# Optimization experiments

Hardware: AMD Instinct MI355X
Metric: run time of the kernel (lower is better)

The kernel has to match this reference:

```python
import jax, jax.numpy as jnp
import numpy as np

HEADS = 8
DIM_HEAD = 64
SCALE = 10.0
EPS = 1e-12  # F.normalize eps


def setup_inputs() -> dict:
    key = jax.random.key(0)
    k1, k2, k3, k4 = jax.random.split(key, 4)
    dim, hidden = 256, HEADS * DIM_HEAD
    x = jax.random.normal(k1, (8, dim, 32, 32), dtype=jnp.float32)
    w_qkv = jax.random.normal(k2, (3 * hidden, dim), dtype=jnp.float32) * (1.0 / np.sqrt(dim))
    w_out = jax.random.normal(k3, (dim, hidden), dtype=jnp.float32) * (1.0 / np.sqrt(hidden))
    b_out = jax.random.normal(k4, (dim,), dtype=jnp.float32) * 0.01
    return {"x": x, "w_qkv": w_qkv, "w_out": w_out, "b_out": b_out}


def _l2norm_last(t):
    # matches F.normalize(t, dim=-1): t / max(||t||_2, eps)
    n = jnp.sqrt(jnp.sum(t * t, axis=-1, keepdims=True))
    return t / jnp.maximum(n, EPS)


def reference(x, w_qkv, w_out, b_out):
    b, c, hh, ww = x.shape
    n = hh * ww
    # 1x1 conv == channel matmul
    qkv = jnp.einsum('bcxy,oc->boxy', x, w_qkv)  # (b, 3*hidden, h, w)
    q, k, v = jnp.split(qkv, 3, axis=1)
    # 'b (h c) x y -> b h c (x y)'
    to_heads = lambda t: t.reshape(b, HEADS, DIM_HEAD, n)
    q, k, v = to_heads(q), to_heads(k), to_heads(v)
    # NOTE: l2norm over the LAST axis = spatial token axis n (faithful to source)
    q = _l2norm_last(q)
    k = _l2norm_last(k)
    sim = jnp.einsum('bhdi,bhdj->bhij', q, k) * SCALE  # (b, h, n, n)
    attn = jax.nn.softmax(sim, axis=-1)
    out = jnp.einsum('bhij,bhdj->bhid', attn, v)  # (b, h, n, d)
    # 'b h (x y) d -> b (h d) x y'
    out = out.transpose(0, 1, 3, 2).reshape(b, HEADS * DIM_HEAD, hh, ww)
    return jnp.einsum('bcxy,oc->boxy', out, w_out) + b_out[None, :, None, None]
```

## Files before the change

kernel.cpp:

```cpp
#include <hip/hip_runtime.h>
#include <math.h>

#define NHEADS 8
#define DHEAD  64
#define HIDDEN 512
#define CIN    256
#define NTOK   1024
#define QK_SCALE 10.0f
#define LOG2E 1.44269504088896f
#define MSHIFT 10.5f
#define MBIAS  (-MSHIFT * LOG2E)

typedef __bf16 bf16x8 __attribute__((ext_vector_type(8)));
typedef float  f32x4  __attribute__((ext_vector_type(4)));
typedef unsigned u32x4 __attribute__((ext_vector_type(4)));
typedef unsigned short u16x8 __attribute__((ext_vector_type(8)));
typedef unsigned short u16x4 __attribute__((ext_vector_type(4)));

__device__ inline unsigned short f2bf(float f) {
    unsigned u = __builtin_bit_cast(unsigned, f);
    u = (u + 0x7FFFu + ((u >> 16) & 1u)) >> 16;
    return (unsigned short)u;
}

__device__ inline unsigned pk2(float a, float b) {
    return (unsigned)f2bf(a) | ((unsigned)f2bf(b) << 16);
}

__device__ inline unsigned pk2t(float a, float b) {
    return (__builtin_bit_cast(unsigned, a) >> 16) |
           (__builtin_bit_cast(unsigned, b) & 0xFFFF0000u);
}
__device__ inline float trunc_bf(float f) {
    return __builtin_bit_cast(float, __builtin_bit_cast(unsigned, f) & 0xFFFF0000u);
}

__device__ inline float bf2f(unsigned short u) {
    return __builtin_bit_cast(float, (unsigned)u << 16);
}

__device__ inline bf16x8 cvt8(const float* p) {
    float4 a = *(const float4*)p;
    float4 b = *(const float4*)(p + 4);
    u16x8 t;
    t[0] = f2bf(a.x); t[1] = f2bf(a.y); t[2] = f2bf(a.z); t[3] = f2bf(a.w);
    t[4] = f2bf(b.x); t[5] = f2bf(b.y); t[6] = f2bf(b.z); t[7] = f2bf(b.w);
    return __builtin_bit_cast(bf16x8, t);
}

__global__ __launch_bounds__(256)
void cvt_x_kernel(const float* __restrict__ x, unsigned short* __restrict__ xt) {
    const int b  = blockIdx.z;
    const int c0 = blockIdx.y * 64;
    const int n0 = blockIdx.x * 64;
    const float* src = x + ((size_t)b * CIN + c0) * NTOK + n0;
    unsigned short* dst = xt + ((size_t)b * NTOK + n0) * CIN + c0;

    __shared__ float T[64][65];
    const int t = threadIdx.x;
    {
        const int nq = t & 15, cg = t >> 4;
        #pragma unroll
        for (int rr = 0; rr < 4; ++rr) {
            const int c = cg + rr * 16;
            float4 v = *(const float4*)(src + (size_t)c * NTOK + nq * 4);
            T[c][nq * 4 + 0] = v.x;
            T[c][nq * 4 + 1] = v.y;
            T[c][nq * 4 + 2] = v.z;
            T[c][nq * 4 + 3] = v.w;
        }
    }
    __syncthreads();
    {
        const int n = t >> 2, cq = t & 3;
        alignas(16) unsigned short tmp[16];
        #pragma unroll
        for (int e = 0; e < 16; ++e)
            tmp[e] = f2bf(T[cq * 16 + e][n]);
        *(uint4*)(dst + (size_t)n * CIN + cq * 16)     = *(uint4*)&tmp[0];
        *(uint4*)(dst + (size_t)n * CIN + cq * 16 + 8) = *(uint4*)&tmp[8];
    }
}

__global__ __launch_bounds__(256)
void cvt_w_kernel(const float* __restrict__ wq, const float* __restrict__ wo,
                  unsigned short* __restrict__ wqb, unsigned short* __restrict__ wob) {
    const size_t i = ((size_t)blockIdx.x * 256 + threadIdx.x) * 8;
    if (i < (size_t)1536 * 256) {
        *(bf16x8*)(wqb + i) = cvt8(wq + i);
    } else {
        const size_t j = i - (size_t)1536 * 256;
        *(bf16x8*)(wob + j) = cvt8(wo + j);
    }
}

__global__ __launch_bounds__(256)
void gemm1_kernel(const unsigned short* __restrict__ wqb,
                  const unsigned short* __restrict__ xt,
                  float* __restrict__ qt,
                  unsigned short* __restrict__ vb,
                  float* __restrict__ ss) {
    const int b  = blockIdx.z;
    const int bm = blockIdx.y * 128;
    const int bn = blockIdx.x * 128;
    const int wave = threadIdx.x >> 6, lane = threadIdx.x & 63;
    const int lo = lane & 15, hi = lane >> 4;
    const int wm = bm + (wave >> 1) * 64;
    const int wn = bn + (wave & 1) * 64;

    const unsigned short* Ab = wqb + (size_t)(wm + lo) * CIN + hi * 8;
    const unsigned short* Bb = xt + ((size_t)b * NTOK + wn + lo) * CIN + hi * 8;

    f32x4 acc[4][4];
    #pragma unroll
    for (int mi = 0; mi < 4; ++mi)
        #pragma unroll
        for (int ni = 0; ni < 4; ++ni) acc[mi][ni] = (f32x4){0.f, 0.f, 0.f, 0.f};

    for (int k0 = 0; k0 < CIN; k0 += 32) {
        bf16x8 a[4], bf[4];
        #pragma unroll
        for (int mi = 0; mi < 4; ++mi) a[mi]  = *(const bf16x8*)(Ab + (size_t)mi * 16 * CIN + k0);
        #pragma unroll
        for (int ni = 0; ni < 4; ++ni) bf[ni] = *(const bf16x8*)(Bb + (size_t)ni * 16 * CIN + k0);
        #pragma unroll
        for (int mi = 0; mi < 4; ++mi)
            #pragma unroll
            for (int ni = 0; ni < 4; ++ni)
                acc[mi][ni] = __builtin_amdgcn_mfma_f32_16x16x32_bf16(a[mi], bf[ni], acc[mi][ni], 0, 0, 0);
    }

    __shared__ unsigned short VL[4][32][72];

    if (bm < 1024) {
        const int isK = (wm >= 512) ? 1 : 0;
        const int ch0 = wm & 511;
        const int head = ch0 >> 6;
        float* dst = qt + (((size_t)isK * 64 + b * 8 + head) * NTOK) * DHEAD;
        #pragma unroll
        for (int mi = 0; mi < 4; ++mi) {
            const int d = mi * 16 + hi * 4;
            #pragma unroll
            for (int ni = 0; ni < 4; ++ni) {
                const int n = wn + ni * 16 + lo;
                *(f32x4*)(dst + (size_t)n * DHEAD + d) = acc[mi][ni];
            }
        }
        float p[4][4];
        #pragma unroll
        for (int mi = 0; mi < 4; ++mi)
            #pragma unroll
            for (int r = 0; r < 4; ++r) {
                float s = 0.f;
                #pragma unroll
                for (int ni = 0; ni < 4; ++ni) s += acc[mi][ni][r] * acc[mi][ni][r];
                p[mi][r] = s;
            }
        #pragma unroll
        for (int off = 1; off < 16; off <<= 1)
            #pragma unroll
            for (int mi = 0; mi < 4; ++mi)
                #pragma unroll
                for (int r = 0; r < 4; ++r)
                    p[mi][r] += __shfl_xor(p[mi][r], off, 64);
        if (lo == 0) {
            #pragma unroll
            for (int mi = 0; mi < 4; ++mi)
                #pragma unroll
                for (int r = 0; r < 4; ++r)
                    atomicAdd(&ss[(size_t)b * 1024 + isK * 512 + ch0 + mi * 16 + hi * 4 + r], p[mi][r]);
        }
    } else {
        const int ch0 = wm - 1024;
        const int h = ch0 >> 6;
        unsigned short* tile = vb + (((size_t)b * 8 + h) * 16 + (wn >> 6)) * 4096;
        #pragma unroll
        for (int half = 0; half < 2; ++half) {
            #pragma unroll
            for (int mm = 0; mm < 2; ++mm) {
                const int mi = half * 2 + mm;
                #pragma unroll
                for (int ni = 0; ni < 4; ++ni)
                    #pragma unroll
                    for (int r = 0; r < 4; ++r)
                        VL[wave][mm * 16 + hi * 4 + r][ni * 16 + lo] = f2bf(acc[mi][ni][r]);
            }
            #pragma unroll
            for (int i = 0; i < 4; ++i) {
                const int flat = i * 64 + lane;
                const int row = flat >> 3, c = flat & 7;
                const int tb = c >> 2, hg = c & 3;
                const uint2 vlo = *(uint2*)&VL[wave][row][tb * 32 + hg * 4];
                const uint2 vhi = *(uint2*)&VL[wave][row][tb * 32 + hg * 4 + 16];
                uint4 v = make_uint4(vlo.x, vlo.y, vhi.x, vhi.y);
                const int d = half * 32 + row;
                *(uint4*)(tile + (size_t)d * 64 + c * 8) = v;
            }
        }
    }
}

__global__ __launch_bounds__(256)
void scale_cvt_kernel(const float* __restrict__ qt, const float* __restrict__ ss,
                      unsigned short* __restrict__ qs, unsigned short* __restrict__ ks) {
    const size_t idx = ((size_t)blockIdx.x * 256 + threadIdx.x) * 8;
    const size_t half = (size_t)64 * NTOK * DHEAD;
    const int isK = idx >= half;
    const size_t rem = idx - (size_t)isK * half;
    const int bh = (int)(rem >> 16);
    const int d0 = (int)(rem & 63);
    const int b  = bh >> 3;
    const int ch = isK * 512 + (bh & 7) * 64 + d0;
    const float scl = isK ? 1.0f : QK_SCALE;

    const float* ip = qt + idx;
    float4 v0 = *(const float4*)ip;
    float4 v1 = *(const float4*)(ip + 4);
    float4 q0 = *(const float4*)(ss + (size_t)b * 1024 + ch);
    float4 q1 = *(const float4*)(ss + (size_t)b * 1024 + ch + 4);
    float4 s0, s1;
    s0.x = 1.0f / fmaxf(sqrtf(q0.x), 1e-12f); s0.y = 1.0f / fmaxf(sqrtf(q0.y), 1e-12f);
    s0.z = 1.0f / fmaxf(sqrtf(q0.z), 1e-12f); s0.w = 1.0f / fmaxf(sqrtf(q0.w), 1e-12f);
    s1.x = 1.0f / fmaxf(sqrtf(q1.x), 1e-12f); s1.y = 1.0f / fmaxf(sqrtf(q1.y), 1e-12f);
    s1.z = 1.0f / fmaxf(sqrtf(q1.z), 1e-12f); s1.w = 1.0f / fmaxf(sqrtf(q1.w), 1e-12f);
    u16x8 t;
    t[0] = f2bf(v0.x * s0.x * scl); t[1] = f2bf(v0.y * s0.y * scl);
    t[2] = f2bf(v0.z * s0.z * scl); t[3] = f2bf(v0.w * s0.w * scl);
    t[4] = f2bf(v1.x * s1.x * scl); t[5] = f2bf(v1.y * s1.y * scl);
    t[6] = f2bf(v1.z * s1.z * scl); t[7] = f2bf(v1.w * s1.w * scl);
    *(u16x8*)((isK ? ks : qs) + rem) = t;
}

__global__ __launch_bounds__(128)
void attn_mfma_kernel(const unsigned short* __restrict__ qs,
                      const unsigned short* __restrict__ ks,
                      const unsigned short* __restrict__ vb,
                      unsigned short* __restrict__ attn_t) {
    const int hw = blockIdx.x;
    const int virt = (hw & 7) * 128 + (hw >> 3);
    const int bh = virt >> 4;
    const int it = virt & 15;
    const int b = bh >> 3, h = bh & 7;

    const int lane = threadIdx.x & 63;
    const int wave = threadIdx.x >> 6;
    const int lo = lane & 15;
    const int hi = lane >> 4;
    const int iw = it * 64 + wave * 32;

    const unsigned short* qbh = qs + (size_t)bh * NTOK * DHEAD;
    const unsigned short* kbh = ks + (size_t)bh * NTOK * DHEAD;
    const unsigned short* vbh = vb + (size_t)bh * 16 * 4096;

    bf16x8 aQ[2][2];
    #pragma unroll
    for (int f = 0; f < 2; ++f) {
        const unsigned short* qp = qbh + (size_t)(iw + f * 16 + lo) * DHEAD + hi * 8;
        aQ[f][0] = *(const bf16x8*)qp;
        aQ[f][1] = *(const bf16x8*)(qp + 32);
    }

    float lsum4[2][4];
    #pragma unroll
    for (int f = 0; f < 2; ++f)
        #pragma unroll
        for (int r = 0; r < 4; ++r) lsum4[f][r] = 0.0f;
    f32x4 acc[2][4];
    #pragma unroll
    for (int f = 0; f < 2; ++f)
        #pragma unroll
        for (int ds = 0; ds < 4; ++ds) acc[f][ds] = (f32x4){0.f, 0.f, 0.f, 0.f};

    #pragma unroll 2
    for (int jt = 0; jt < 16; ++jt) {
        const int j0 = jt * 64;

        bf16x8 bV[4][2];
        {
            const unsigned short* vt = vbh + (size_t)jt * 4096;
            #pragma unroll
            for (int ds = 0; ds < 4; ++ds) {
                const unsigned short* vp = vt + (ds * 16 + lo) * 64 + hi * 8;
                bV[ds][0] = *(const bf16x8*)vp;
                bV[ds][1] = *(const bf16x8*)(vp + 32);
            }
        }

        bf16x8 bK[4][2];
        #pragma unroll
        for (int jj = 0; jj < 4; ++jj) {
            const unsigned short* kp = kbh + (size_t)(j0 + jj * 16 + lo) * DHEAD + hi * 8;
            bK[jj][0] = *(const bf16x8*)kp;
            bK[jj][1] = *(const bf16x8*)(kp + 32);
        }

        f32x4 s[2][4];
        __builtin_amdgcn_s_setprio(1);
        #pragma unroll
        for (int jj = 0; jj < 4; ++jj)
            #pragma unroll
            for (int f = 0; f < 2; ++f) {
                f32x4 c = (f32x4){0.f, 0.f, 0.f, 0.f};
                c = __builtin_amdgcn_mfma_f32_16x16x32_bf16(bK[jj][0], aQ[f][0], c, 0, 0, 0);
                c = __builtin_amdgcn_mfma_f32_16x16x32_bf16(bK[jj][1], aQ[f][1], c, 0, 0, 0);
                s[f][jj] = c;
            }
        __builtin_amdgcn_s_setprio(0);

        unsigned pw[2][2][4];
        #pragma unroll
        for (int f = 0; f < 2; ++f) {
            #pragma unroll
            for (int jj = 0; jj < 4; ++jj)
                #pragma unroll
                for (int r = 0; r < 4; ++r) {
                    const float p = __builtin_amdgcn_exp2f(fmaf(s[f][jj][r], LOG2E, MBIAS));
                    s[f][jj][r] = p;
                    lsum4[f][r] += trunc_bf(p);
                }
            #pragma unroll
            for (int t = 0; t < 2; ++t) {
                pw[f][t][0] = pk2t(s[f][2 * t][0],     s[f][2 * t][1]);
                pw[f][t][1] = pk2t(s[f][2 * t][2],     s[f][2 * t][3]);
                pw[f][t][2] = pk2t(s[f][2 * t + 1][0], s[f][2 * t + 1][1]);
                pw[f][t][3] = pk2t(s[f][2 * t + 1][2], s[f][2 * t + 1][3]);
            }
        }

        __builtin_amdgcn_s_setprio(1);
        #pragma unroll
        for (int ds = 0; ds < 4; ++ds)
            #pragma unroll
            for (int f = 0; f < 2; ++f)
                #pragma unroll
                for (int t = 0; t < 2; ++t) {
                    const bf16x8 bp = __builtin_bit_cast(bf16x8,
                        (u32x4){pw[f][t][0], pw[f][t][1], pw[f][t][2], pw[f][t][3]});
                    acc[f][ds] = __builtin_amdgcn_mfma_f32_16x16x32_bf16(bV[ds][t], bp, acc[f][ds], 0, 0, 0);
                }
        __builtin_amdgcn_s_setprio(0);
    }

    float lsum[2];
    #pragma unroll
    for (int f = 0; f < 2; ++f) {
        lsum[f] = (lsum4[f][0] + lsum4[f][1]) + (lsum4[f][2] + lsum4[f][3]);
        lsum[f] += __shfl_xor(lsum[f], 16, 64);
        lsum[f] += __shfl_xor(lsum[f], 32, 64);
    }

    unsigned short* at = attn_t + ((size_t)b * NTOK + iw) * HIDDEN + h * DHEAD;
    #pragma unroll
    for (int f = 0; f < 2; ++f) {
        const float inv = 1.0f / lsum[f];
        #pragma unroll
        for (int ds = 0; ds < 4; ++ds) {
            uint2 w;
            w.x = pk2(acc[f][ds][0] * inv, acc[f][ds][1] * inv);
            w.y = pk2(acc[f][ds][2] * inv, acc[f][ds][3] * inv);
            *(uint2*)(at + (size_t)(f * 16 + lo) * HIDDEN + ds * 16 + hi * 4) = w;
        }
    }
}

__global__ __launch_bounds__(128)
void gemm2_kernel(const unsigned short* __restrict__ wob,
                  const unsigned short* __restrict__ attn_t,
                  const float* __restrict__ b_out,
                  float* __restrict__ out) {
    const int b  = blockIdx.z;
    const int bm = blockIdx.y * 64;
    const int bn = blockIdx.x * 128;
    const int wave = threadIdx.x >> 6, lane = threadIdx.x & 63;
    const int lo = lane & 15, hi = lane >> 4;
    const int wn = bn + wave * 64;

    const unsigned short* Ab = wob + (size_t)(bm + lo) * HIDDEN + hi * 8;
    const unsigned short* Bb = attn_t + ((size_t)b * NTOK + wn + lo) * HIDDEN + hi * 8;

    f32x4 acc[4][4];
    #pragma unroll
    for (int mi = 0; mi < 4; ++mi)
        #pragma unroll
        for (int ni = 0; ni < 4; ++ni) acc[mi][ni] = (f32x4){0.f, 0.f, 0.f, 0.f};

    for (int k0 = 0; k0 < HIDDEN; k0 += 32) {
        bf16x8 a[4], bf[4];
        #pragma unroll
        for (int mi = 0; mi < 4; ++mi) a[mi]  = *(const bf16x8*)(Ab + (size_t)mi * 16 * HIDDEN + k0);
        #pragma unroll
        for (int ni = 0; ni < 4; ++ni) bf[ni] = *(const bf16x8*)(Bb + (size_t)ni * 16 * HIDDEN + k0);
        #pragma unroll
        for (int mi = 0; mi < 4; ++mi)
            #pragma unroll
            for (int ni = 0; ni < 4; ++ni)
                acc[mi][ni] = __builtin_amdgcn_mfma_f32_16x16x32_bf16(a[mi], bf[ni], acc[mi][ni], 0, 0, 0);
    }

    __shared__ float OL[2][32][69];
    #pragma unroll
    for (int half = 0; half < 2; ++half) {
        #pragma unroll
        for (int mm = 0; mm < 2; ++mm) {
            const int mi = half * 2 + mm;
            #pragma unroll
            for (int ni = 0; ni < 4; ++ni)
                #pragma unroll
                for (int r = 0; r < 4; ++r)
                    OL[wave][mm * 16 + hi * 4 + r][ni * 16 + lo] = acc[mi][ni][r];
        }
        #pragma unroll
        for (int i = 0; i < 8; ++i) {
            const int flat = i * 64 + lane;
            const int row = flat >> 4, c = flat & 15;
            float4 v = *(float4*)&OL[wave][row][c * 4];
            const int m = bm + half * 32 + row;
            const float bb = b_out[m];
            v.x += bb; v.y += bb; v.z += bb; v.w += bb;
            *(float4*)(out + ((size_t)b * CIN + m) * NTOK + wn + c * 4) = v;
        }
    }
}

extern "C" void kernel_launch(void* const* d_in, const int* in_sizes, int n_in,
                              void* d_out, int out_size, void* d_ws, size_t ws_size,
                              hipStream_t stream) {
    const float* x     = (const float*)d_in[0];
    const float* w_qkv = (const float*)d_in[1];
    const float* w_out = (const float*)d_in[2];
    const float* b_out = (const float*)d_in[3];
    float* out = (float*)d_out;

    char* ws = (char*)d_ws;
    unsigned short* xt  = (unsigned short*)(ws);
    unsigned short* wqb = (unsigned short*)(ws + 4194304);
    unsigned short* wob = (unsigned short*)(ws + 4980736);
    float*          ss  = (float*)(ws + 5242880);
    unsigned short* qs  = (unsigned short*)(ws + 5308416);
    unsigned short* ks  = (unsigned short*)(ws + 13697024);
    unsigned short* vb  = (unsigned short*)(ws + 22085632);
    float*          qt  = (float*)(ws + 30474240);
    unsigned short* attn_t = (unsigned short*)(ws + 30474240);

    hipMemsetAsync(ss, 0, 8 * 1024 * sizeof(float), stream);

    cvt_x_kernel<<<dim3(16, 4, 8), 256, 0, stream>>>(x, xt);
    cvt_w_kernel<<<256, 256, 0, stream>>>(w_qkv, w_out, wqb, wob);

    gemm1_kernel<<<dim3(8, 12, 8), 256, 0, stream>>>(wqb, xt, qt, vb, ss);

    scale_cvt_kernel<<<4096, 256, 0, stream>>>(qt, ss, qs, ks);

    attn_mfma_kernel<<<1024, 128, 0, stream>>>(qs, ks, vb, attn_t);

    gemm2_kernel<<<dim3(8, 4, 8), 128, 0, stream>>>(wob, attn_t, b_out, out);
}
```

Before: 196.9 us.

## Fold q/k normalization into attention Q scaling and merge prep kernels

Gemm1 now writes unnormalized Q/K as bf16 instead of fp32, and the full-size scale_cvt pass is replaced by a tiny kernel that computes one combined per-channel factor, scale/(|q|·|k|). The attention kernel applies that factor to the Q fragments on load. The x and weight conversion kernels are merged into one launch. The softmax row sum is now computed with an extra MFMA against a ones vector instead of per-element VALU adds and shuffles. Together these remove a large fp32 round trip and a launch, at the cost of Q/K being rounded to bf16 before normalization and an extra bf16 rounding when the scale is applied.

```diff
diff --git a/kernel.cpp b/kernel.cpp
--- a/kernel.cpp
+++ b/kernel.cpp
@@ -15,7 +15,6 @@
 typedef float  f32x4  __attribute__((ext_vector_type(4)));
 typedef unsigned u32x4 __attribute__((ext_vector_type(4)));
 typedef unsigned short u16x8 __attribute__((ext_vector_type(8)));
-typedef unsigned short u16x4 __attribute__((ext_vector_type(4)));
 
 __device__ inline unsigned short f2bf(float f) {
     unsigned u = __builtin_bit_cast(unsigned, f);
@@ -30,9 +29,6 @@
 __device__ inline unsigned pk2t(float a, float b) {
     return (__builtin_bit_cast(unsigned, a) >> 16) |
            (__builtin_bit_cast(unsigned, b) & 0xFFFF0000u);
-}
-__device__ inline float trunc_bf(float f) {
-    return __builtin_bit_cast(float, __builtin_bit_cast(unsigned, f) & 0xFFFF0000u);
 }
 
 __device__ inline float bf2f(unsigned short u) {
@@ -48,56 +44,67 @@
     return __builtin_bit_cast(bf16x8, t);
 }
 
+__device__ inline bf16x8 scale8(bf16x8 v, const float* s) {
+    u16x8 u = __builtin_bit_cast(u16x8, v);
+    u32x4 r;
+    r[0] = pk2(bf2f(u[0]) * s[0], bf2f(u[1]) * s[1]);
+    r[1] = pk2(bf2f(u[2]) * s[2], bf2f(u[3]) * s[3]);
+    r[2] = pk2(bf2f(u[4]) * s[4], bf2f(u[5]) * s[5]);
+    r[3] = pk2(bf2f(u[6]) * s[6], bf2f(u[7]) * s[7]);
+    return __builtin_bit_cast(bf16x8, r);
+}
+
 __global__ __launch_bounds__(256)
-void cvt_x_kernel(const float* __restrict__ x, unsigned short* __restrict__ xt) {
-    const int b  = blockIdx.z;
-    const int c0 = blockIdx.y * 64;
-    const int n0 = blockIdx.x * 64;
-    const float* src = x + ((size_t)b * CIN + c0) * NTOK + n0;
-    unsigned short* dst = xt + ((size_t)b * NTOK + n0) * CIN + c0;
-
+void prep_kernel(const float* __restrict__ x, const float* __restrict__ wq,
+                 const float* __restrict__ wo,
+                 unsigned short* __restrict__ xt, unsigned short* __restrict__ wqb,
+                 unsigned short* __restrict__ wob) {
     __shared__ float T[64][65];
+    const int blk = blockIdx.x;
     const int t = threadIdx.x;
-    {
-        const int nq = t & 15, cg = t >> 4;
-        #pragma unroll
-        for (int rr = 0; rr < 4; ++rr) {
-            const int c = cg + rr * 16;
-            float4 v = *(const float4*)(src + (size_t)c * NTOK + nq * 4);
-            T[c][nq * 4 + 0] = v.x;
-            T[c][nq * 4 + 1] = v.y;
-            T[c][nq * 4 + 2] = v.z;
-            T[c][nq * 4 + 3] = v.w;
-        }
-    }
-    __syncthreads();
-    {
-        const int n = t >> 2, cq = t & 3;
-        alignas(16) unsigned short tmp[16];
-        #pragma unroll
-        for (int e = 0; e < 16; ++e)
-            tmp[e] = f2bf(T[cq * 16 + e][n]);
-        *(uint4*)(dst + (size_t)n * CIN + cq * 16)     = *(uint4*)&tmp[0];
-        *(uint4*)(dst + (size_t)n * CIN + cq * 16 + 8) = *(uint4*)&tmp[8];
-    }
-}
-
-__global__ __launch_bounds__(256)
-void cvt_w_kernel(const float* __restrict__ wq, const float* __restrict__ wo,
-                  unsigned short* __restrict__ wqb, unsigned short* __restrict__ wob) {
-    const size_t i = ((size_t)blockIdx.x * 256 + threadIdx.x) * 8;
-    if (i < (size_t)1536 * 256) {
-        *(bf16x8*)(wqb + i) = cvt8(wq + i);
+    if (blk < 512) {
+        const int n0 = (blk & 15) * 64;
+        const int c0 = ((blk >> 4) & 3) * 64;
+        const int b  = blk >> 6;
+        const float* src = x + ((size_t)b * CIN + c0) * NTOK + n0;
+        unsigned short* dst = xt + ((size_t)b * NTOK + n0) * CIN + c0;
+        {
+            const int nq = t & 15, cg = t >> 4;
+            #pragma unroll
+            for (int rr = 0; rr < 4; ++rr) {
+                const int c = cg + rr * 16;
+                float4 v = *(const float4*)(src + (size_t)c * NTOK + nq * 4);
+                T[c][nq * 4 + 0] = v.x;
+                T[c][nq * 4 + 1] = v.y;
+                T[c][nq * 4 + 2] = v.z;
+                T[c][nq * 4 + 3] = v.w;
+            }
+        }
+        __syncthreads();
+        {
+            const int n = t >> 2, cq = t & 3;
+            alignas(16) unsigned short tmp[16];
+            #pragma unroll
+            for (int e = 0; e < 16; ++e)
+                tmp[e] = f2bf(T[cq * 16 + e][n]);
+            *(uint4*)(dst + (size_t)n * CIN + cq * 16)     = *(uint4*)&tmp[0];
+            *(uint4*)(dst + (size_t)n * CIN + cq * 16 + 8) = *(uint4*)&tmp[8];
+        }
     } else {
-        const size_t j = i - (size_t)1536 * 256;
-        *(bf16x8*)(wob + j) = cvt8(wo + j);
+        const size_t i = ((size_t)(blk - 512) * 256 + t) * 8;
+        if (i < (size_t)1536 * 256) {
+            *(bf16x8*)(wqb + i) = cvt8(wq + i);
+        } else {
+            const size_t j = i - (size_t)1536 * 256;
+            *(bf16x8*)(wob + j) = cvt8(wo + j);
+        }
     }
 }
 
 __global__ __launch_bounds__(256)
 void gemm1_kernel(const unsigned short* __restrict__ wqb,
                   const unsigned short* __restrict__ xt,
-                  float* __restrict__ qt,
+                  unsigned short* __restrict__ qk,
                   unsigned short* __restrict__ vb,
                   float* __restrict__ ss) {
     const int b  = blockIdx.z;
@@ -136,14 +143,17 @@
         const int isK = (wm >= 512) ? 1 : 0;
         const int ch0 = wm & 511;
         const int head = ch0 >> 6;
-        float* dst = qt + (((size_t)isK * 64 + b * 8 + head) * NTOK) * DHEAD;
+        unsigned short* dst = qk + (((size_t)(isK * 64 + b * 8 + head)) * NTOK) * DHEAD;
         #pragma unroll
         for (int mi = 0; mi < 4; ++mi) {
             const int d = mi * 16 + hi * 4;
             #pragma unroll
             for (int ni = 0; ni < 4; ++ni) {
                 const int n = wn + ni * 16 + lo;
-                *(f32x4*)(dst + (size_t)n * DHEAD + d) = acc[mi][ni];
+                uint2 wv;
+                wv.x = pk2(acc[mi][ni][0], acc[mi][ni][1]);
+                wv.y = pk2(acc[mi][ni][2], acc[mi][ni][3]);
+                *(uint2*)(dst + (size_t)n * DHEAD + d) = wv;
             }
         }
         float p[4][4];
@@ -201,40 +211,18 @@
 }
 
 __global__ __launch_bounds__(256)
-void scale_cvt_kernel(const float* __restrict__ qt, const float* __restrict__ ss,
-                      unsigned short* __restrict__ qs, unsigned short* __restrict__ ks) {
-    const size_t idx = ((size_t)blockIdx.x * 256 + threadIdx.x) * 8;
-    const size_t half = (size_t)64 * NTOK * DHEAD;
-    const int isK = idx >= half;
-    const size_t rem = idx - (size_t)isK * half;
-    const int bh = (int)(rem >> 16);
-    const int d0 = (int)(rem & 63);
-    const int b  = bh >> 3;
-    const int ch = isK * 512 + (bh & 7) * 64 + d0;
-    const float scl = isK ? 1.0f : QK_SCALE;
-
-    const float* ip = qt + idx;
-    float4 v0 = *(const float4*)ip;
-    float4 v1 = *(const float4*)(ip + 4);
-    float4 q0 = *(const float4*)(ss + (size_t)b * 1024 + ch);
-    float4 q1 = *(const float4*)(ss + (size_t)b * 1024 + ch + 4);
-    float4 s0, s1;
-    s0.x = 1.0f / fmaxf(sqrtf(q0.x), 1e-12f); s0.y = 1.0f / fmaxf(sqrtf(q0.y), 1e-12f);
-    s0.z = 1.0f / fmaxf(sqrtf(q0.z), 1e-12f); s0.w = 1.0f / fmaxf(sqrtf(q0.w), 1e-12f);
-    s1.x = 1.0f / fmaxf(sqrtf(q1.x), 1e-12f); s1.y = 1.0f / fmaxf(sqrtf(q1.y), 1e-12f);
-    s1.z = 1.0f / fmaxf(sqrtf(q1.z), 1e-12f); s1.w = 1.0f / fmaxf(sqrtf(q1.w), 1e-12f);
-    u16x8 t;
-    t[0] = f2bf(v0.x * s0.x * scl); t[1] = f2bf(v0.y * s0.y * scl);
-    t[2] = f2bf(v0.z * s0.z * scl); t[3] = f2bf(v0.w * s0.w * scl);
-    t[4] = f2bf(v1.x * s1.x * scl); t[5] = f2bf(v1.y * s1.y * scl);
-    t[6] = f2bf(v1.z * s1.z * scl); t[7] = f2bf(v1.w * s1.w * scl);
-    *(u16x8*)((isK ? ks : qs) + rem) = t;
+void wnorm_kernel(const float* __restrict__ ss, float* __restrict__ wsc) {
+    const int i = blockIdx.x * 256 + threadIdx.x;
+    const int b = i >> 9, ch = i & 511;
+    const float nq = fmaxf(sqrtf(ss[(size_t)b * 1024 + ch]),       1e-12f);
+    const float nk = fmaxf(sqrtf(ss[(size_t)b * 1024 + 512 + ch]), 1e-12f);
+    wsc[i] = QK_SCALE / (nq * nk);
 }
 
 __global__ __launch_bounds__(128)
-void attn_mfma_kernel(const unsigned short* __restrict__ qs,
-                      const unsigned short* __restrict__ ks,
+void attn_mfma_kernel(const unsigned short* __restrict__ qk,
                       const unsigned short* __restrict__ vb,
+                      const float* __restrict__ wsc,
                       unsigned short* __restrict__ attn_t) {
     const int hw = blockIdx.x;
     const int virt = (hw & 7) * 128 + (hw >> 3);
@@ -248,28 +236,38 @@
     const int hi = lane >> 4;
     const int iw = it * 64 + wave * 32;
 
-    const unsigned short* qbh = qs + (size_t)bh * NTOK * DHEAD;
-    const unsigned short* kbh = ks + (size_t)bh * NTOK * DHEAD;
+    const unsigned short* qbh = qk + (size_t)bh * NTOK * DHEAD;
+    const unsigned short* kbh = qk + (size_t)(64 + bh) * NTOK * DHEAD;
     const unsigned short* vbh = vb + (size_t)bh * 16 * 4096;
+
+    float wa[8], wb[8];
+    {
+        const float* wp = wsc + (size_t)b * 512 + h * DHEAD;
+        *(float4*)&wa[0] = *(const float4*)(wp + hi * 8);
+        *(float4*)&wa[4] = *(const float4*)(wp + hi * 8 + 4);
+        *(float4*)&wb[0] = *(const float4*)(wp + 32 + hi * 8);
+        *(float4*)&wb[4] = *(const float4*)(wp + 32 + hi * 8 + 4);
+    }
 
     bf16x8 aQ[2][2];
     #pragma unroll
     for (int f = 0; f < 2; ++f) {
         const unsigned short* qp = qbh + (size_t)(iw + f * 16 + lo) * DHEAD + hi * 8;
-        aQ[f][0] = *(const bf16x8*)qp;
-        aQ[f][1] = *(const bf16x8*)(qp + 32);
-    }
-
-    float lsum4[2][4];
-    #pragma unroll
-    for (int f = 0; f < 2; ++f)
-        #pragma unroll
-        for (int r = 0; r < 4; ++r) lsum4[f][r] = 0.0f;
+        aQ[f][0] = scale8(*(const bf16x8*)qp,        wa);
+        aQ[f][1] = scale8(*(const bf16x8*)(qp + 32), wb);
+    }
+
+    const bf16x8 ones = __builtin_bit_cast(bf16x8,
+        (u32x4){0x3F803F80u, 0x3F803F80u, 0x3F803F80u, 0x3F803F80u});
+
     f32x4 acc[2][4];
-    #pragma unroll
-    for (int f = 0; f < 2; ++f)
+    f32x4 accl[2];
+    #pragma unroll
+    for (int f = 0; f < 2; ++f) {
+        accl[f] = (f32x4){0.f, 0.f, 0.f, 0.f};
         #pragma unroll
         for (int ds = 0; ds < 4; ++ds) acc[f][ds] = (f32x4){0.f, 0.f, 0.f, 0.f};
+    }
 
     #pragma unroll 2
     for (int jt = 0; jt < 16; ++jt) {
@@ -307,52 +305,42 @@
             }
         __builtin_amdgcn_s_setprio(0);
 
-        unsigned pw[2][2][4];
+        bf16x8 bp[2][2];
         #pragma unroll
         for (int f = 0; f < 2; ++f) {
             #pragma unroll
             for (int jj = 0; jj < 4; ++jj)
                 #pragma unroll
-                for (int r = 0; r < 4; ++r) {
-                    const float p = __builtin_amdgcn_exp2f(fmaf(s[f][jj][r], LOG2E, MBIAS));
-                    s[f][jj][r] = p;
-                    lsum4[f][r] += trunc_bf(p);
-                }
+                for (int r = 0; r < 4; ++r)
+                    s[f][jj][r] = __builtin_amdgcn_exp2f(fmaf(s[f][jj][r], LOG2E, MBIAS));
             #pragma unroll
             for (int t = 0; t < 2; ++t) {
-                pw[f][t][0] = pk2t(s[f][2 * t][0],     s[f][2 * t][1]);
-                pw[f][t][1] = pk2t(s[f][2 * t][2],     s[f][2 * t][3]);
-                pw[f][t][2] = pk2t(s[f][2 * t + 1][0], s[f][2 * t + 1][1]);
-                pw[f][t][3] = pk2t(s[f][2 * t + 1][2], s[f][2 * t + 1][3]);
+                u32x4 pw;
+                pw[0] = pk2t(s[f][2 * t][0],     s[f][2 * t][1]);
+                pw[1] = pk2t(s[f][2 * t][2],     s[f][2 * t][3]);
+                pw[2] = pk2t(s[f][2 * t + 1][0], s[f][2 * t + 1][1]);
+                pw[3] = pk2t(s[f][2 * t + 1][2], s[f][2 * t + 1][3]);
+                bp[f][t] = __builtin_bit_cast(bf16x8, pw);
             }
         }
 
         __builtin_amdgcn_s_setprio(1);
         #pragma unroll
-        for (int ds = 0; ds < 4; ++ds)
-            #pragma unroll
-            for (int f = 0; f < 2; ++f)
-                #pragma unroll
-                for (int t = 0; t < 2; ++t) {
-                    const bf16x8 bp = __builtin_bit_cast(bf16x8,
-                        (u32x4){pw[f][t][0], pw[f][t][1], pw[f][t][2], pw[f][t][3]});
-                    acc[f][ds] = __builtin_amdgcn_mfma_f32_16x16x32_bf16(bV[ds][t], bp, acc[f][ds], 0, 0, 0);
-                }
+        for (int f = 0; f < 2; ++f)
+            #pragma unroll
+            for (int t = 0; t < 2; ++t) {
+                accl[f] = __builtin_amdgcn_mfma_f32_16x16x32_bf16(ones, bp[f][t], accl[f], 0, 0, 0);
+                #pragma unroll
+                for (int ds = 0; ds < 4; ++ds)
+                    acc[f][ds] = __builtin_amdgcn_mfma_f32_16x16x32_bf16(bV[ds][t], bp[f][t], acc[f][ds], 0, 0, 0);
+            }
         __builtin_amdgcn_s_setprio(0);
     }
 
-    float lsum[2];
+    unsigned short* at = attn_t + ((size_t)b * NTOK + iw) * HIDDEN + h * DHEAD;
     #pragma unroll
     for (int f = 0; f < 2; ++f) {
-        lsum[f] = (lsum4[f][0] + lsum4[f][1]) + (lsum4[f][2] + lsum4[f][3]);
-        lsum[f] += __shfl_xor(lsum[f], 16, 64);
-        lsum[f] += __shfl_xor(lsum[f], 32, 64);
-    }
-
-    unsigned short* at = attn_t + ((size_t)b * NTOK + iw) * HIDDEN + h * DHEAD;
-    #pragma unroll
-    for (int f = 0; f < 2; ++f) {
-        const float inv = 1.0f / lsum[f];
+        const float inv = 1.0f / accl[f][0];
         #pragma unroll
         for (int ds = 0; ds < 4; ++ds) {
             uint2 w;
@@ -436,22 +424,20 @@
     unsigned short* wqb = (unsigned short*)(ws + 4194304);
     unsigned short* wob = (unsigned short*)(ws + 4980736);
     float*          ss  = (float*)(ws + 5242880);
-    unsigned short* qs  = (unsigned short*)(ws + 5308416);
-    unsigned short* ks  = (unsigned short*)(ws + 13697024);
-    unsigned short* vb  = (unsigned short*)(ws + 22085632);
-    float*          qt  = (float*)(ws + 30474240);
-    unsigned short* attn_t = (unsigned short*)(ws + 30474240);
+    float*          wsc = (float*)(ws + 5275648);
+    unsigned short* qk  = (unsigned short*)(ws + 5292032);
+    unsigned short* vb  = (unsigned short*)(ws + 22069248);
+    unsigned short* attn_t = (unsigned short*)(ws + 30457856);
 
     hipMemsetAsync(ss, 0, 8 * 1024 * sizeof(float), stream);
 
-    cvt_x_kernel<<<dim3(16, 4, 8), 256, 0, stream>>>(x, xt);
-    cvt_w_kernel<<<256, 256, 0, stream>>>(w_qkv, w_out, wqb, wob);
-
-    gemm1_kernel<<<dim3(8, 12, 8), 256, 0, stream>>>(wqb, xt, qt, vb, ss);
-
-    scale_cvt_kernel<<<4096, 256, 0, stream>>>(qt, ss, qs, ks);
-
-    attn_mfma_kernel<<<1024, 128, 0, stream>>>(qs, ks, vb, attn_t);
+    prep_kernel<<<768, 256, 0, stream>>>(x, w_qkv, w_out, xt, wqb, wob);
+
+    gemm1_kernel<<<dim3(8, 12, 8), 256, 0, stream>>>(wqb, xt, qk, vb, ss);
+
+    wnorm_kernel<<<16, 256, 0, stream>>>(ss, wsc);
+
+    attn_mfma_kernel<<<1024, 128, 0, stream>>>(qk, vb, wsc, attn_t);
 
     gemm2_kernel<<<dim3(8, 4, 8), 128, 0, stream>>>(wob, attn_t, b_out, out);
 }
```

Result: faster. 179.3 us (-8.9%).
